# Kernel optimization log

Hardware: AMD Instinct MI355X
Metric: run time of the kernel (lower is better)

## Reference

```python
import jax, jax.numpy as jnp
import numpy as np

N, K, D = 65536, 1024, 256

def setup_inputs() -> dict:
    key = jax.random.key(0)
    k1, k2 = jax.random.split(key)
    inputs = jax.random.normal(k1, (N, D), dtype=jnp.float32)
    # keras 'random_uniform' initializer: U(-0.05, 0.05)
    clusters = jax.random.uniform(k2, (K, D), dtype=jnp.float32, minval=-0.05, maxval=0.05)
    return {"inputs": inputs, "clusters": clusters}

def reference(inputs, clusters):
    # argmin over squared distances == argmin over tf.norm (sqrt is monotonic),
    # so the returned gathered centroids are identical to the original module.
    x2 = jnp.sum(inputs * inputs, axis=1, keepdims=True)          # [N,1]
    c2 = jnp.sum(clusters * clusters, axis=1)                      # [K]
    xc = jnp.einsum('nd,kd->nk', inputs, clusters)                # [N,K]
    d2 = x2 - 2.0 * xc + c2[None, :]                               # [N,K]
    assignments = jnp.argmin(d2, axis=1)                           # [N]
    return clusters[assignments]                                   # [N,D]
```

## Files before the change

### kernel.cpp

```cpp
#include <hip/hip_runtime.h>

#define K_CL  1024
#define D_DIM 256
#define BN    128
#define CTILE 128
#define NCT   (K_CL / CTILE)

typedef __attribute__((ext_vector_type(8))) short bf16x8;
typedef __attribute__((ext_vector_type(4))) float f32x4;

__device__ __forceinline__ short f2bf(float f) {
    unsigned b = __float_as_uint(f);
    unsigned r = (b + 0x7FFFu + ((b >> 16) & 1u)) >> 16;
    return (short)r;
}

__device__ __forceinline__ void gload_lds16(const void* g, void* l) {
    __builtin_amdgcn_global_load_lds(
        (const __attribute__((address_space(1))) unsigned int*)g,
        (__attribute__((address_space(3))) unsigned int*)l, 16, 0, 0);
}

template <typename F>
__device__ float np_pairwise_half(F ld, int base4) {
#pragma clang fp contract(off)
    float4 f0 = ld(base4 + 0);
    float4 f1 = ld(base4 + 1);
    float r0 = __fmul_rn(f0.x, f0.x), r1 = __fmul_rn(f0.y, f0.y);
    float r2 = __fmul_rn(f0.z, f0.z), r3 = __fmul_rn(f0.w, f0.w);
    float r4 = __fmul_rn(f1.x, f1.x), r5 = __fmul_rn(f1.y, f1.y);
    float r6 = __fmul_rn(f1.z, f1.z), r7 = __fmul_rn(f1.w, f1.w);
    #pragma unroll
    for (int p = 1; p < 16; ++p) {
        float4 a = ld(base4 + 2 * p);
        float4 b = ld(base4 + 2 * p + 1);
        r0 = __fadd_rn(r0, __fmul_rn(a.x, a.x)); r1 = __fadd_rn(r1, __fmul_rn(a.y, a.y));
        r2 = __fadd_rn(r2, __fmul_rn(a.z, a.z)); r3 = __fadd_rn(r3, __fmul_rn(a.w, a.w));
        r4 = __fadd_rn(r4, __fmul_rn(b.x, b.x)); r5 = __fadd_rn(r5, __fmul_rn(b.y, b.y));
        r6 = __fadd_rn(r6, __fmul_rn(b.z, b.z)); r7 = __fadd_rn(r7, __fmul_rn(b.w, b.w));
    }
    return __fadd_rn(__fadd_rn(__fadd_rn(r0, r1), __fadd_rn(r2, r3)),
                     __fadd_rn(__fadd_rn(r4, r5), __fadd_rn(r6, r7)));
}

__global__ void prep_kernel(const float* __restrict__ C, short* __restrict__ Cs,
                            float* __restrict__ c2) {
#pragma clang fp contract(off)
    int d    = blockIdx.x * 256 + threadIdx.x;
    int n    = d >> 9;
    int r    = d & 511;
    int ks   = r >> 6;
    int kg   = (r >> 4) & 3;
    int lo   = r & 15;
    int col  = n * 16 + lo;
    const float* src = C + (size_t)col * D_DIM + ks * 32 + kg * 8;
    float4 a = *reinterpret_cast<const float4*>(src);
    float4 b = *reinterpret_cast<const float4*>(src + 4);
    bf16x8 o;
    o[0] = f2bf(a.x); o[1] = f2bf(a.y); o[2] = f2bf(a.z); o[3] = f2bf(a.w);
    o[4] = f2bf(b.x); o[5] = f2bf(b.y); o[6] = f2bf(b.z); o[7] = f2bf(b.w);
    reinterpret_cast<bf16x8*>(Cs)[d] = o;

    if (blockIdx.x < 8) {
        int id   = blockIdx.x * 128 + (threadIdx.x >> 1);
        int half = threadIdx.x & 1;
        const float4* row = reinterpret_cast<const float4*>(C) + (size_t)id * 64;
        auto ld = [&](int d4) { return row[d4]; };
        float v = np_pairwise_half(ld, half * 32);
        float other = __shfl_xor(v, 1);
        if (half == 0) c2[id] = __fadd_rn(v, other);
    }
}

__launch_bounds__(256, 2)
__global__ void kmeans_fused(const float* __restrict__ X, const float* __restrict__ C,
                             const short* __restrict__ Cswz, const float* __restrict__ c2g,
                             float* __restrict__ out) {
#pragma clang fp contract(off)
    __shared__ bf16x8   Bs[CTILE * 32];
    __shared__ float    c2s[K_CL];
    __shared__ float    x2L[BN];
    __shared__ unsigned candL[BN][4];
    __shared__ int      asgL[BN];
    __shared__ int      needL[BN];
    __shared__ int      cntL;

    const int tid  = threadIdx.x;
    const int w    = tid >> 6;
    const int l    = tid & 63;
    const int lo16 = l & 15;
    const int kg   = l >> 4;
    const int blk_row0  = blockIdx.x * BN;
    const int wave_row0 = blk_row0 + w * 32;

    const bf16x8* Cs8 = reinterpret_cast<const bf16x8*>(Cswz);

    if (tid == 0) cntL = 0;

    #pragma unroll
    for (int i = 0; i < 4; ++i) c2s[tid + i * 256] = __fadd_rn(c2g[tid + i * 256], 32.0f);

    bf16x8 af[2][8];
    #pragma unroll
    for (int m = 0; m < 2; ++m)
        #pragma unroll
        for (int ks = 0; ks < 8; ++ks) {
            const float* xr = X + (size_t)(wave_row0 + m * 16 + lo16) * D_DIM + ks * 32 + kg * 8;
            float4 u = *reinterpret_cast<const float4*>(xr);
            float4 v = *reinterpret_cast<const float4*>(xr + 4);
            bf16x8 o;
            o[0] = f2bf(u.x); o[1] = f2bf(u.y); o[2] = f2bf(u.z); o[3] = f2bf(u.w);
            o[4] = f2bf(v.x); o[5] = f2bf(v.y); o[6] = f2bf(v.z); o[7] = f2bf(v.w);
            af[m][ks] = o;
        }

    {
        int r = l >> 1, half = l & 1;
        const float4* xr4 = reinterpret_cast<const float4*>(X + (size_t)(wave_row0 + r) * D_DIM);
        auto ld = [&](int d4) { return xr4[d4]; };
        float v = np_pairwise_half(ld, half * 32);
        float other = __shfl_xor(v, 1);
        if (half == 0) x2L[w * 32 + r] = __fadd_rn(v, other);
    }

    unsigned t[2][4][2];
    #pragma unroll
    for (int m = 0; m < 2; ++m)
        #pragma unroll
        for (int j = 0; j < 4; ++j) { t[m][j][0] = 0xFFFFFFFFu; t[m][j][1] = 0xFFFFFFFFu; }

    f32x4 a0p = {-1e30f, -1e30f, -1e30f, -1e30f};
    f32x4 a1p = a0p;
    int   colp = lo16;

    #define INSERT_PREV() { \
        float ccp = c2s[colp]; \
        _Pragma("unroll") \
        for (int m = 0; m < 2; ++m) { \
            _Pragma("unroll") \
            for (int j = 0; j < 4; ++j) { \
                float s2 = fmaf(-2.0f, (m == 0 ? a0p[j] : a1p[j]), ccp); \
                unsigned p = (__float_as_uint(s2) & 0xFFFFFC00u) | (unsigned)colp; \
                unsigned o1 = min(t[m][j][1], max(p, t[m][j][0])); \
                unsigned o0 = min(t[m][j][0], p); \
                t[m][j][1] = o1; t[m][j][0] = o0; \
            } \
        } }

    for (int Tc = 0; Tc < NCT; ++Tc) {
        __syncthreads();
        {
            const bf16x8* gsrc = Cs8 + (size_t)Tc * (CTILE * 32);
            #pragma unroll
            for (int c = 0; c < 16; ++c)
                gload_lds16(&gsrc[c * 256 + tid], &Bs[c * 256 + tid]);
        }
        __syncthreads();

        #pragma unroll
        for (int s = 0; s < 8; ++s) {
            int n = Tc * 8 + s;
            bf16x8 bfv[8];
            #pragma unroll
            for (int ks = 0; ks < 8; ++ks)
                bfv[ks] = Bs[s * 512 + ks * 64 + kg * 16 + lo16];
            f32x4 p0 = {0.f,0.f,0.f,0.f}, p1 = {0.f,0.f,0.f,0.f};
            f32x4 q0 = {0.f,0.f,0.f,0.f}, q1 = {0.f,0.f,0.f,0.f};
            #pragma unroll
            for (int ks = 0; ks < 4; ++ks) {
                p0 = __builtin_amdgcn_mfma_f32_16x16x32_bf16(af[0][ks],     bfv[ks],     p0, 0, 0, 0);
                q0 = __builtin_amdgcn_mfma_f32_16x16x32_bf16(af[1][ks],     bfv[ks],     q0, 0, 0, 0);
                p1 = __builtin_amdgcn_mfma_f32_16x16x32_bf16(af[0][ks + 4], bfv[ks + 4], p1, 0, 0, 0);
                q1 = __builtin_amdgcn_mfma_f32_16x16x32_bf16(af[1][ks + 4], bfv[ks + 4], q1, 0, 0, 0);
            }
            INSERT_PREV();
            a0p = p0 + p1;
            a1p = q0 + q1;
            colp = n * 16 + lo16;
        }
    }
    INSERT_PREV();
    #undef INSERT_PREV

    #pragma unroll
    for (int m = 0; m < 2; ++m)
        #pragma unroll
        for (int j = 0; j < 4; ++j) {
            unsigned v0 = t[m][j][0], v1 = t[m][j][1];
            unsigned v2 = 0xFFFFFFFFu, v3 = 0xFFFFFFFFu;
            #pragma unroll
            for (int mask = 1; mask <= 8; mask <<= 1) {
                unsigned o0 = (unsigned)__shfl_xor((int)v0, mask);
                unsigned o1 = (unsigned)__shfl_xor((int)v1, mask);
                unsigned o2 = (unsigned)__shfl_xor((int)v2, mask);
                unsigned o3 = (unsigned)__shfl_xor((int)v3, mask);
                unsigned c0 = min(v0, o3), c1 = min(v1, o2), c2_ = min(v2, o1), c3 = min(v3, o0);
                unsigned lo, hi;
                lo = min(c0, c2_); hi = max(c0, c2_); c0 = lo; c2_ = hi;
                lo = min(c1, c3);  hi = max(c1, c3);  c1 = lo; c3  = hi;
                lo = min(c0, c1);  hi = max(c0, c1);  c0 = lo; c1  = hi;
                lo = min(c2_, c3); hi = max(c2_, c3); c2_ = lo; c3 = hi;
                v0 = c0; v1 = c1; v2 = c2_; v3 = c3;
            }
            if (lo16 == 0) {
                int rl  = m * 16 + kg * 4 + j;
                int row = w * 32 + rl;
                candL[row][0] = v0 & 1023u;
                candL[row][1] = v1 & 1023u;
                candL[row][2] = v2 & 1023u;
                candL[row][3] = v3 & 1023u;
                float g = __fsub_rn(__uint_as_float(v1 & 0xFFFFFC00u),
                                    __uint_as_float(v0 & 0xFFFFFC00u));
                if (g >= 0.06f) {
                    asgL[row] = (int)(v0 & 1023u);
                } else {
                    int slot = atomicAdd(&cntL, 1);
                    needL[slot] = row;
                }
            }
        }
    __syncthreads();

    {
        int M = cntL;
        #pragma unroll
        for (int slot = 0; slot < 2; ++slot) {
            int id = slot * 256 + tid;
            if (id < 4 * M) {
                int rr   = needL[id >> 2];
                int c    = id & 3;
                int cand = (int)candL[rr][c];
                const float4* xr4 = reinterpret_cast<const float4*>(X + (size_t)(blk_row0 + rr) * D_DIM);
                const float4* cr4 = reinterpret_cast<const float4*>(C + (size_t)cand * D_DIM);
                float acc = 0.0f;
                #pragma unroll 8
                for (int d4 = 0; d4 < 64; ++d4) {
                    float4 xv = xr4[d4], cv = cr4[d4];
                    acc = __fadd_rn(acc, __fmul_rn(xv.x, cv.x));
                    acc = __fadd_rn(acc, __fmul_rn(xv.y, cv.y));
                    acc = __fadd_rn(acc, __fmul_rn(xv.z, cv.z));
                    acc = __fadd_rn(acc, __fmul_rn(xv.w, cv.w));
                }
                float sc = __fadd_rn(__fsub_rn(x2L[rr], __fmul_rn(2.0f, acc)), c2g[cand]);
                #pragma unroll
                for (int mm = 1; mm <= 2; mm <<= 1) {
                    float os = __shfl_xor(sc, mm);
                    int   oc = __shfl_xor(cand, mm);
                    if (os < sc || (os == sc && oc < cand)) { sc = os; cand = oc; }
                }
                if (c == 0) asgL[rr] = cand;
            }
        }
    }
    __syncthreads();

    const f32x4* C4 = reinterpret_cast<const f32x4*>(C);
    f32x4* O4 = reinterpret_cast<f32x4*>(out) + (size_t)blk_row0 * 64;
    #pragma unroll
    for (int i = 0; i < 32; ++i) {
        int flat = tid + i * 256;
        int r    = flat >> 6;
        int d4   = flat & 63;
        f32x4 v = C4[(size_t)asgL[r] * 64 + d4];
        __builtin_nontemporal_store(v, &O4[flat]);
    }
}

extern "C" void kernel_launch(void* const* d_in, const int* in_sizes, int n_in,
                              void* d_out, int out_size, void* d_ws, size_t ws_size,
                              hipStream_t stream) {
    const float* X = (const float*)d_in[0];
    const float* C = (const float*)d_in[1];
    float* out = (float*)d_out;

    char* ws = (char*)d_ws;
    float* c2 = (float*)ws;
    short* Cs = (short*)(ws + 4096);

    int N = in_sizes[0] / D_DIM;

    prep_kernel<<<(K_CL * D_DIM / 8) / 256, 256, 0, stream>>>(C, Cs, c2);
    kmeans_fused<<<N / BN, 256, 0, stream>>>(X, C, Cs, c2, out);
}
```

Baseline: 73.07 us.

## Split centroid tile work across two wave groups per block with top-4 merge

```diff
diff --git a/kernel.cpp b/kernel.cpp
--- a/kernel.cpp
+++ b/kernel.cpp
@@ -72,7 +72,7 @@
     }
 }
 
-__launch_bounds__(256, 2)
+__launch_bounds__(512, 4)
 __global__ void kmeans_fused(const float* __restrict__ X, const float* __restrict__ C,
                              const short* __restrict__ Cswz, const float* __restrict__ c2g,
                              float* __restrict__ out) {
@@ -80,6 +80,7 @@
     __shared__ bf16x8   Bs[CTILE * 32];
     __shared__ float    c2s[K_CL];
     __shared__ float    x2L[BN];
+    __shared__ unsigned cand8L[BN][8];
     __shared__ unsigned candL[BN][4];
     __shared__ int      asgL[BN];
     __shared__ int      needL[BN];
@@ -87,18 +88,20 @@
 
     const int tid  = threadIdx.x;
     const int w    = tid >> 6;
+    const int wsub = w & 3;
+    const int half = w >> 2;
     const int l    = tid & 63;
     const int lo16 = l & 15;
     const int kg   = l >> 4;
     const int blk_row0  = blockIdx.x * BN;
-    const int wave_row0 = blk_row0 + w * 32;
+    const int wave_row0 = blk_row0 + wsub * 32;
 
     const bf16x8* Cs8 = reinterpret_cast<const bf16x8*>(Cswz);
 
     if (tid == 0) cntL = 0;
 
     #pragma unroll
-    for (int i = 0; i < 4; ++i) c2s[tid + i * 256] = __fadd_rn(c2g[tid + i * 256], 32.0f);
+    for (int i = 0; i < 2; ++i) c2s[tid + i * 512] = __fadd_rn(c2g[tid + i * 512], 32.0f);
 
     bf16x8 af[2][8];
     #pragma unroll
@@ -114,13 +117,13 @@
             af[m][ks] = o;
         }
 
-    {
-        int r = l >> 1, half = l & 1;
+    if (half == 0) {
+        int r = l >> 1, hh = l & 1;
         const float4* xr4 = reinterpret_cast<const float4*>(X + (size_t)(wave_row0 + r) * D_DIM);
         auto ld = [&](int d4) { return xr4[d4]; };
-        float v = np_pairwise_half(ld, half * 32);
+        float v = np_pairwise_half(ld, hh * 32);
         float other = __shfl_xor(v, 1);
-        if (half == 0) x2L[w * 32 + r] = __fadd_rn(v, other);
+        if (hh == 0) x2L[wsub * 32 + r] = __fadd_rn(v, other);
     }
 
     unsigned t[2][4][2];
@@ -152,18 +155,19 @@
         {
             const bf16x8* gsrc = Cs8 + (size_t)Tc * (CTILE * 32);
             #pragma unroll
-            for (int c = 0; c < 16; ++c)
-                gload_lds16(&gsrc[c * 256 + tid], &Bs[c * 256 + tid]);
+            for (int c = 0; c < 8; ++c)
+                gload_lds16(&gsrc[c * 512 + tid], &Bs[c * 512 + tid]);
         }
         __syncthreads();
 
         #pragma unroll
-        for (int s = 0; s < 8; ++s) {
-            int n = Tc * 8 + s;
+        for (int s = 0; s < 4; ++s) {
+            int sp = half * 4 + s;
+            int n  = Tc * 8 + sp;
             bf16x8 bfv[8];
             #pragma unroll
             for (int ks = 0; ks < 8; ++ks)
-                bfv[ks] = Bs[s * 512 + ks * 64 + kg * 16 + lo16];
+                bfv[ks] = Bs[sp * 512 + ks * 64 + kg * 16 + lo16];
             f32x4 p0 = {0.f,0.f,0.f,0.f}, p1 = {0.f,0.f,0.f,0.f};
             f32x4 q0 = {0.f,0.f,0.f,0.f}, q1 = {0.f,0.f,0.f,0.f};
             #pragma unroll
@@ -203,53 +207,70 @@
                 v0 = c0; v1 = c1; v2 = c2_; v3 = c3;
             }
             if (lo16 == 0) {
-                int rl  = m * 16 + kg * 4 + j;
-                int row = w * 32 + rl;
-                candL[row][0] = v0 & 1023u;
-                candL[row][1] = v1 & 1023u;
-                candL[row][2] = v2 & 1023u;
-                candL[row][3] = v3 & 1023u;
-                float g = __fsub_rn(__uint_as_float(v1 & 0xFFFFFC00u),
-                                    __uint_as_float(v0 & 0xFFFFFC00u));
-                if (g >= 0.06f) {
-                    asgL[row] = (int)(v0 & 1023u);
-                } else {
-                    int slot = atomicAdd(&cntL, 1);
-                    needL[slot] = row;
-                }
+                int row = wsub * 32 + m * 16 + kg * 4 + j;
+                cand8L[row][half * 4 + 0] = v0;
+                cand8L[row][half * 4 + 1] = v1;
+                cand8L[row][half * 4 + 2] = v2;
+                cand8L[row][half * 4 + 3] = v3;
             }
         }
     __syncthreads();
 
+    if (tid < BN) {
+        int rr = tid;
+        unsigned A0 = cand8L[rr][0], A1 = cand8L[rr][1], A2 = cand8L[rr][2], A3 = cand8L[rr][3];
+        unsigned B0 = cand8L[rr][4], B1 = cand8L[rr][5], B2 = cand8L[rr][6], B3 = cand8L[rr][7];
+        unsigned Av[4] = {A0, A1, A2, A3};
+        unsigned Bv[4] = {B0, B1, B2, B3};
+        unsigned outv[4];
+        int i = 0, j = 0;
+        #pragma unroll
+        for (int k = 0; k < 4; ++k) {
+            unsigned av = (i < 4) ? Av[i] : 0xFFFFFFFFu;
+            unsigned bv = (j < 4) ? Bv[j] : 0xFFFFFFFFu;
+            if (av <= bv) { outv[k] = av; ++i; } else { outv[k] = bv; ++j; }
+        }
+        candL[rr][0] = outv[0] & 1023u;
+        candL[rr][1] = outv[1] & 1023u;
+        candL[rr][2] = outv[2] & 1023u;
+        candL[rr][3] = outv[3] & 1023u;
+        float g = __fsub_rn(__uint_as_float(outv[1] & 0xFFFFFC00u),
+                            __uint_as_float(outv[0] & 0xFFFFFC00u));
+        if (g >= 0.06f) {
+            asgL[rr] = (int)(outv[0] & 1023u);
+        } else {
+            int slot = atomicAdd(&cntL, 1);
+            needL[slot] = rr;
+        }
+    }
+    __syncthreads();
+
     {
-        int M = cntL;
-        #pragma unroll
-        for (int slot = 0; slot < 2; ++slot) {
-            int id = slot * 256 + tid;
-            if (id < 4 * M) {
-                int rr   = needL[id >> 2];
-                int c    = id & 3;
-                int cand = (int)candL[rr][c];
-                const float4* xr4 = reinterpret_cast<const float4*>(X + (size_t)(blk_row0 + rr) * D_DIM);
-                const float4* cr4 = reinterpret_cast<const float4*>(C + (size_t)cand * D_DIM);
-                float acc = 0.0f;
-                #pragma unroll 8
-                for (int d4 = 0; d4 < 64; ++d4) {
-                    float4 xv = xr4[d4], cv = cr4[d4];
-                    acc = __fadd_rn(acc, __fmul_rn(xv.x, cv.x));
-                    acc = __fadd_rn(acc, __fmul_rn(xv.y, cv.y));
-                    acc = __fadd_rn(acc, __fmul_rn(xv.z, cv.z));
-                    acc = __fadd_rn(acc, __fmul_rn(xv.w, cv.w));
-                }
-                float sc = __fadd_rn(__fsub_rn(x2L[rr], __fmul_rn(2.0f, acc)), c2g[cand]);
-                #pragma unroll
-                for (int mm = 1; mm <= 2; mm <<= 1) {
-                    float os = __shfl_xor(sc, mm);
-                    int   oc = __shfl_xor(cand, mm);
-                    if (os < sc || (os == sc && oc < cand)) { sc = os; cand = oc; }
-                }
-                if (c == 0) asgL[rr] = cand;
-            }
+        int M4 = 4 * cntL;
+        int id = tid;
+        if (id < M4) {
+            int rr   = needL[id >> 2];
+            int c    = id & 3;
+            int cand = (int)candL[rr][c];
+            const float4* xr4 = reinterpret_cast<const float4*>(X + (size_t)(blk_row0 + rr) * D_DIM);
+            const float4* cr4 = reinterpret_cast<const float4*>(C + (size_t)cand * D_DIM);
+            float acc = 0.0f;
+            #pragma unroll 8
+            for (int d4 = 0; d4 < 64; ++d4) {
+                float4 xv = xr4[d4], cv = cr4[d4];
+                acc = __fadd_rn(acc, __fmul_rn(xv.x, cv.x));
+                acc = __fadd_rn(acc, __fmul_rn(xv.y, cv.y));
+                acc = __fadd_rn(acc, __fmul_rn(xv.z, cv.z));
+                acc = __fadd_rn(acc, __fmul_rn(xv.w, cv.w));
+            }
+            float sc = __fadd_rn(__fsub_rn(x2L[rr], __fmul_rn(2.0f, acc)), c2g[cand]);
+            #pragma unroll
+            for (int mm = 1; mm <= 2; mm <<= 1) {
+                float os = __shfl_xor(sc, mm);
+                int   oc = __shfl_xor(cand, mm);
+                if (os < sc || (os == sc && oc < cand)) { sc = os; cand = oc; }
+            }
+            if (c == 0) asgL[rr] = cand;
         }
     }
     __syncthreads();
@@ -257,8 +278,8 @@
     const f32x4* C4 = reinterpret_cast<const f32x4*>(C);
     f32x4* O4 = reinterpret_cast<f32x4*>(out) + (size_t)blk_row0 * 64;
     #pragma unroll
-    for (int i = 0; i < 32; ++i) {
-        int flat = tid + i * 256;
+    for (int i = 0; i < 16; ++i) {
+        int flat = tid + i * 512;
         int r    = flat >> 6;
         int d4   = flat & 63;
         f32x4 v = C4[(size_t)asgL[r] * 64 + d4];
@@ -280,5 +301,5 @@
     int N = in_sizes[0] / D_DIM;
 
     prep_kernel<<<(K_CL * D_DIM / 8) / 256, 256, 0, stream>>>(C, Cs, c2);
-    kmeans_fused<<<N / BN, 256, 0, stream>>>(X, C, Cs, c2, out);
-}
+    kmeans_fused<<<N / BN, 512, 0, stream>>>(X, C, Cs, c2, out);
+}
```

Result: slower. 182.4 us (+149.6%).
